# Kernel tuning notes

Hardware: AMD Instinct MI355X
Metric: run time of the kernel (lower is better)

Reference implementation:

```python
import jax, jax.numpy as jnp
import numpy as np

H = 90          # hidden size
T = 240         # timesteps
F = 180         # encoder input features (3*60)


def _lstmcell_zero_state(x, W_ih, b_ih, b_hh):
    """nn.LSTMCell applied with h0=c0=0 (as in the original loops).
    x: [..., in_feat]; W_ih: [4H, in_feat]. Gate order i,f,g,o (PyTorch)."""
    gates = jnp.einsum('btf,gf->btg', x, W_ih) + b_ih + b_hh  # [B,T,4H]
    i, f, g, o = jnp.split(gates, 4, axis=-1)
    c = jax.nn.sigmoid(i) * jnp.tanh(g)          # f * c0 term vanishes (c0=0)
    return jax.nn.sigmoid(o) * jnp.tanh(c)       # h'


def setup_inputs() -> dict:
    key = jax.random.key(0)
    ks = jax.random.split(key, 9)
    s_enc = 1.0 / np.sqrt(H)
    inp = {
        'x': jax.random.normal(ks[0], (1024, 3, 60, T), dtype=jnp.float32),
        'enc_W_ih': jax.random.uniform(ks[1], (4 * H, F), jnp.float32, -s_enc, s_enc),
        'enc_b_ih': jax.random.uniform(ks[2], (4 * H,), jnp.float32, -s_enc, s_enc),
        'enc_b_hh': jax.random.uniform(ks[3], (4 * H,), jnp.float32, -s_enc, s_enc),
        'dec_W_ih': jax.random.uniform(ks[4], (4 * H, H), jnp.float32, -s_enc, s_enc),
        'dec_b_ih': jax.random.uniform(ks[5], (4 * H,), jnp.float32, -s_enc, s_enc),
        'dec_b_hh': jax.random.uniform(ks[6], (4 * H,), jnp.float32, -s_enc, s_enc),
        'out_W': jax.random.uniform(ks[7], (40, T * H), jnp.float32, -1.0 / np.sqrt(T * H), 1.0 / np.sqrt(T * H)),
        'out_b': jax.random.uniform(ks[8], (40,), jnp.float32, -1.0 / np.sqrt(T * H), 1.0 / np.sqrt(T * H)),
    }
    return inp


def reference(x, enc_W_ih, enc_b_ih, enc_b_hh, dec_W_ih, dec_b_ih, dec_b_hh, out_W, out_b):
    # Encoder: [B,3,60,240] -> [B,240,180]
    xe = jnp.transpose(x, (0, 3, 1, 2)).reshape(-1, T, F)
    h1 = jax.nn.sigmoid(_lstmcell_zero_state(xe, enc_W_ih, enc_b_ih, enc_b_hh))  # [B,T,90]
    # Decoder: per-step LSTMCell (also zero-state each step)
    h2 = _lstmcell_zero_state(h1, dec_W_ih, dec_b_ih, dec_b_hh)  # [B,T,90]
    out = h2.reshape(-1, T * H) @ out_W.T + out_b                # [B,40]
    out = out.reshape(-1, 4, 10)
    return jax.nn.softmax(out, axis=2)
```

## Files before the change

kernel.cpp:

```cpp
#include <hip/hip_runtime.h>
#include <hip/hip_bf16.h>

#define TT 240
#define FEAT 180
#define HID 90

typedef __attribute__((ext_vector_type(8))) short bf16x8;
typedef __attribute__((ext_vector_type(4))) short s16x4;
typedef __attribute__((ext_vector_type(4))) float f32x4;

static __device__ __forceinline__ short f2bf(float f) {
    union { float f; unsigned int u; } c; c.f = f;
    return (short)((c.u + 0x8000u) >> 16);
}
static __device__ __forceinline__ float fexp2(float x) { return __builtin_amdgcn_exp2f(x); }
static __device__ __forceinline__ float frcp(float x)  { return __builtin_amdgcn_rcpf(x); }
#define LOG2E 1.4426950408889634f
static __device__ __forceinline__ float sigm(float x)  { return frcp(1.f + fexp2(-LOG2E * x)); }
static __device__ __forceinline__ float tanh_(float x) { return 2.f * frcp(1.f + fexp2(-2.f * LOG2E * x)) - 1.f; }
static __device__ __forceinline__ unsigned int pk2(float lo, float hi) {
    return (unsigned int)(unsigned short)f2bf(lo) | ((unsigned int)(unsigned short)f2bf(hi) << 16);
}

__global__ __launch_bounds__(256) void k_prep(
    const float* __restrict__ outW, const float* __restrict__ encW,
    const float* __restrict__ decW,
    short* __restrict__ woutB, short* __restrict__ wencP, short* __restrict__ wdecP)
{
    int idx = blockIdx.x * 256 + threadIdx.x;
    if (idx < 129600) {
        int row = idx / 2700, v = idx - row * 2700;
        uint4 w = {0u, 0u, 0u, 0u};
        if (row < 40) {
            const float* s = outW + row * 21600 + v * 8;
            f32x4 a = *(const f32x4*)(s);
            f32x4 b = *(const f32x4*)(s + 4);
            w.x = pk2(a[0], a[1]); w.y = pk2(a[2], a[3]);
            w.z = pk2(b[0], b[1]); w.w = pk2(b[2], b[3]);
        }
        *(uint4*)(woutB + row * 21600 + v * 8) = w;
        return;
    }
    idx -= 129600;
    if (idx < 288 * 192) {
        int row = idx / 192, k = idx - row * 192;
        int gi = row / 96, h = row - gi * 96;
        float v = 0.f;
        if (h < 90 && k < 180) {
            int srow = (gi == 0 ? 0 : (gi == 1 ? 180 : 270)) + h;
            v = encW[srow * 180 + k];
        }
        wencP[idx] = f2bf(v);
        return;
    }
    idx -= 288 * 192;
    if (idx < 288 * 96) {
        int row = idx / 96, k = idx - row * 96;
        int gi = row / 96, h = row - gi * 96;
        float v = 0.f;
        if (h < 90 && k < 90) {
            int srow = (gi == 0 ? 0 : (gi == 1 ? 180 : 270)) + h;
            v = decW[srow * 90 + k];
        }
        wdecP[idx] = f2bf(v);
    }
}

__global__ __launch_bounds__(384) void k_ed(
    const float* __restrict__ x,
    const short* __restrict__ wencP, const short* __restrict__ wdecP,
    const float* __restrict__ eb_ih, const float* __restrict__ eb_hh,
    const float* __restrict__ db_ih, const float* __restrict__ db_hh,
    short* __restrict__ h2)
{
    __shared__ short As[64][200];
    const int tid  = threadIdx.x;
    const int lane = tid & 63;
    const int wv   = tid >> 6;
    const int b    = blockIdx.x >> 2;
    const int q    = blockIdx.x & 3;
    const int r15  = lane & 15;
    const int k8   = lane >> 4;
    const int rbase = k8 * 4;

    bf16x8 wfE[3][6];
    #pragma unroll
    for (int g = 0; g < 3; ++g) {
        const short* wp = wencP + (g * 96 + wv * 16 + r15) * 192 + k8 * 8;
        #pragma unroll
        for (int kk = 0; kk < 6; ++kk) wfE[g][kk] = *(const bf16x8*)(wp + kk * 32);
    }
    const int h  = wv * 16 + r15;
    const int hc = (h < 90) ? h : 89;
    const float bIe = eb_ih[hc] + eb_hh[hc];
    const float bGe = eb_ih[180 + hc] + eb_hh[180 + hc];
    const float bOe = eb_ih[270 + hc] + eb_hh[270 + hc];
    const float bId = db_ih[hc] + db_hh[hc];
    const float bGd = db_ih[180 + hc] + db_hh[180 + hc];
    const float bOd = db_ih[270 + hc] + db_hh[270 + hc];

    {
        int row = tid / 6, u = tid - row * 6;
        *(unsigned int*)(&As[row][180 + u * 2]) = 0u;
        if (tid < 360) {
            int r = 60 + tid / 90, c2 = (tid - (tid / 90) * 90) * 2;
            *(unsigned int*)(&As[r][c2]) = 0u;
        }
    }

    {
        const float* xs = x + b * 43200 + q * 60;
        #pragma unroll
        for (int it = 0; it < 2; ++it) {
            int task = tid + 384 * it;
            if (task < 675) {
                int fb = task / 15, v = task - fb * 15;
                const float* p = xs + (fb * 4) * 240 + v * 4;
                f32x4 L0 = *(const f32x4*)(p);
                f32x4 L1 = *(const f32x4*)(p + 240);
                f32x4 L2 = *(const f32x4*)(p + 480);
                f32x4 L3 = *(const f32x4*)(p + 720);
                #pragma unroll
                for (int i = 0; i < 4; ++i) {
                    s16x4 w = { f2bf(L0[i]), f2bf(L1[i]), f2bf(L2[i]), f2bf(L3[i]) };
                    *(s16x4*)(&As[v * 4 + i][fb * 4]) = w;
                }
            }
        }
    }
    __syncthreads();

    short h1v[16];
    #pragma unroll
    for (int rs = 0; rs < 4; ++rs) {
        f32x4 aI = {0.f,0.f,0.f,0.f}, aG = {0.f,0.f,0.f,0.f}, aO = {0.f,0.f,0.f,0.f};
        #pragma unroll
        for (int kk = 0; kk < 6; ++kk) {
            bf16x8 a = *(const bf16x8*)(&As[rs * 16 + r15][kk * 32 + k8 * 8]);
            aI = __builtin_amdgcn_mfma_f32_16x16x32_bf16(a, wfE[0][kk], aI, 0, 0, 0);
            aG = __builtin_amdgcn_mfma_f32_16x16x32_bf16(a, wfE[1][kk], aG, 0, 0, 0);
            aO = __builtin_amdgcn_mfma_f32_16x16x32_bf16(a, wfE[2][kk], aO, 0, 0, 0);
        }
        #pragma unroll
        for (int rg = 0; rg < 4; ++rg) {
            float c  = sigm(aI[rg] + bIe) * tanh_(aG[rg] + bGe);
            float hv = sigm(aO[rg] + bOe) * tanh_(c);
            h1v[rs * 4 + rg] = f2bf(sigm(hv));
        }
    }
    __syncthreads();

    #pragma unroll
    for (int j = 0; j < 16; ++j)
        As[(j >> 2) * 16 + rbase + (j & 3)][h] = h1v[j];

    bf16x8 wfD[3][3];
    #pragma unroll
    for (int g = 0; g < 3; ++g) {
        const short* wp = wdecP + (g * 96 + wv * 16 + r15) * 96 + k8 * 8;
        #pragma unroll
        for (int kk = 0; kk < 3; ++kk) wfD[g][kk] = *(const bf16x8*)(wp + kk * 32);
    }
    __syncthreads();

    short h2v[16];
    #pragma unroll
    for (int rs = 0; rs < 4; ++rs) {
        f32x4 aI = {0.f,0.f,0.f,0.f}, aG = {0.f,0.f,0.f,0.f}, aO = {0.f,0.f,0.f,0.f};
        #pragma unroll
        for (int kk = 0; kk < 3; ++kk) {
            bf16x8 a = *(const bf16x8*)(&As[rs * 16 + r15][kk * 32 + k8 * 8]);
            aI = __builtin_amdgcn_mfma_f32_16x16x32_bf16(a, wfD[0][kk], aI, 0, 0, 0);
            aG = __builtin_amdgcn_mfma_f32_16x16x32_bf16(a, wfD[1][kk], aG, 0, 0, 0);
            aO = __builtin_amdgcn_mfma_f32_16x16x32_bf16(a, wfD[2][kk], aO, 0, 0, 0);
        }
        #pragma unroll
        for (int rg = 0; rg < 4; ++rg) {
            float c  = sigm(aI[rg] + bId) * tanh_(aG[rg] + bGd);
            float o2 = sigm(aO[rg] + bOd) * tanh_(c);
            h2v[rs * 4 + rg] = f2bf(o2);
        }
    }
    __syncthreads();

    short* h2s = &As[0][0];
    #pragma unroll
    for (int j = 0; j < 16; ++j)
        h2s[((j >> 2) * 16 + rbase + (j & 3)) * 96 + h] = h2v[j];
    __syncthreads();

    unsigned int* hp = (unsigned int*)(h2 + (size_t)b * 21600 + q * 5400);
    #pragma unroll
    for (int i = 0; i < 8; ++i) {
        int idx = tid + 384 * i;
        if (idx < 2700) {
            int r = idx / 45, c = idx - r * 45;
            hp[idx] = *(const unsigned int*)(&h2s[r * 96 + c * 2]);
        }
    }
}

#define KSPLIT 45
#define KST    15
__global__ __launch_bounds__(256) void k_out(
    const short* __restrict__ h2, const short* __restrict__ woutB,
    float* __restrict__ part, int B)
{
    __shared__ short Bs[48][488];
    const int MT  = B >> 6;
    const int bid = blockIdx.x;
    const int kc  = bid / MT;
    const int mt  = bid - kc * MT;
    const int tid = threadIdx.x;

    {
        const int k0 = kc * 480;
        #pragma unroll
        for (int j = 0; j < 12; ++j) {
            int g = tid + 256 * j;
            if (g < 2880) {
                int r = g / 60, c = g - r * 60;
                *(uint4*)(&Bs[r][c * 8]) =
                    *(const uint4*)(woutB + (size_t)r * 21600 + k0 + c * 8);
            }
        }
    }
    __syncthreads();

    const int w = tid >> 6, lane = tid & 63;
    const int r15 = lane & 15, k8 = lane >> 4;
    const int row = mt * 64 + w * 16 + r15;
    const short* aB = h2 + (size_t)row * 21600 + kc * 480 + k8 * 8;

    f32x4 a0 = {0.f,0.f,0.f,0.f}, a1 = {0.f,0.f,0.f,0.f}, a2 = {0.f,0.f,0.f,0.f};
    #pragma unroll 5
    for (int ks = 0; ks < KST; ++ks) {
        bf16x8 a  = *(const bf16x8*)(aB + ks * 32);
        bf16x8 q0 = *(const bf16x8*)(&Bs[r15][ks * 32 + k8 * 8]);
        bf16x8 q1 = *(const bf16x8*)(&Bs[16 + r15][ks * 32 + k8 * 8]);
        bf16x8 q2 = *(const bf16x8*)(&Bs[32 + r15][ks * 32 + k8 * 8]);
        a0 = __builtin_amdgcn_mfma_f32_16x16x32_bf16(a, q0, a0, 0, 0, 0);
        a1 = __builtin_amdgcn_mfma_f32_16x16x32_bf16(a, q1, a1, 0, 0, 0);
        a2 = __builtin_amdgcn_mfma_f32_16x16x32_bf16(a, q2, a2, 0, 0, 0);
    }
    float* pb = part + ((size_t)kc * B + mt * 64 + w * 16) * 48;
    #pragma unroll
    for (int rg = 0; rg < 4; ++rg) {
        int r = k8 * 4 + rg;
        pb[r * 48 +      r15] = a0[rg];
        pb[r * 48 + 16 + r15] = a1[rg];
        pb[r * 48 + 32 + r15] = a2[rg];
    }
}

__global__ __launch_bounds__(256) void k_soft(
    const float* __restrict__ part, const float* __restrict__ outb,
    float* __restrict__ out, int B)
{
    const int b = blockIdx.x, tid = threadIdx.x;
    __shared__ float psum[240];
    __shared__ float vals[40];
    if (tid < 240) {
        int o = tid % 40, g = tid / 40;
        float s = 0.f;
        for (int kc = g; kc < KSPLIT; kc += 6)
            s += part[((size_t)kc * B + b) * 48 + o];
        psum[tid] = s;
    }
    __syncthreads();
    if (tid < 40) {
        float s = outb[tid];
        #pragma unroll
        for (int g = 0; g < 6; ++g) s += psum[tid + 40 * g];
        vals[tid] = s;
    }
    __syncthreads();
    if (tid < 4) {
        float mx = -1e30f;
        #pragma unroll
        for (int j = 0; j < 10; ++j) mx = fmaxf(mx, vals[tid * 10 + j]);
        float e[10], s = 0.f;
        #pragma unroll
        for (int j = 0; j < 10; ++j) { e[j] = fexp2(LOG2E * (vals[tid * 10 + j] - mx)); s += e[j]; }
        float inv = frcp(s);
        #pragma unroll
        for (int j = 0; j < 10; ++j) out[b * 40 + tid * 10 + j] = e[j] * inv;
    }
}

extern "C" void kernel_launch(void* const* d_in, const int* in_sizes, int n_in,
                              void* d_out, int out_size, void* d_ws, size_t ws_size,
                              hipStream_t stream)
{
    const float* x     = (const float*)d_in[0];
    const float* encW  = (const float*)d_in[1];
    const float* eb_ih = (const float*)d_in[2];
    const float* eb_hh = (const float*)d_in[3];
    const float* decW  = (const float*)d_in[4];
    const float* db_ih = (const float*)d_in[5];
    const float* db_hh = (const float*)d_in[6];
    const float* outW  = (const float*)d_in[7];
    const float* outb  = (const float*)d_in[8];
    float* out = (float*)d_out;

    const int B = in_sizes[0] / (3 * 60 * TT);

    char* ws = (char*)d_ws;
    short* woutB = (short*)ws;
    short* wencP = (short*)(ws + 2073600);
    short* wdecP = (short*)(ws + 2184192);
    short* h2    = (short*)(ws + 2239488);
    float* part  = (float*)(ws + 2239488 + (size_t)B * 43200);

    k_prep<<<dim3(831), dim3(256), 0, stream>>>(outW, encW, decW, woutB, wencP, wdecP);
    k_ed<<<dim3(B * 4), dim3(384), 0, stream>>>(x, wencP, wdecP, eb_ih, eb_hh,
                                                db_ih, db_hh, h2);
    k_out<<<dim3(KSPLIT * (B >> 6)), dim3(256), 0, stream>>>(h2, woutB, part, B);
    k_soft<<<dim3(B), dim3(256), 0, stream>>>(part, outb, out, B);
}
```

Measured before the change: 361.1 us.

## Make encoder-decoder kernel persistent per batch with double-buffered x staging

k_ed now runs one block per batch element instead of four. It loops over the four 60-step quarters, double-buffering the x tile in LDS so the next quarter's global loads overlap decoder compute, and loads the encoder and decoder weight fragments into registers only once. Decoder outputs are written straight to global memory instead of going through an LDS staging pass. Other changes: hardware v_cvt_pk_bf16_f32 packing, full unroll of the k_out loop, and a vectorised split-K reduction in k_soft. The cost is fewer blocks, which reduces parallelism, plus doubled LDS and higher register pressure.

```diff
diff --git a/kernel.cpp b/kernel.cpp
--- a/kernel.cpp
+++ b/kernel.cpp
@@ -2,25 +2,24 @@
 #include <hip/hip_bf16.h>
 
 #define TT 240
-#define FEAT 180
-#define HID 90
 
 typedef __attribute__((ext_vector_type(8))) short bf16x8;
-typedef __attribute__((ext_vector_type(4))) short s16x4;
 typedef __attribute__((ext_vector_type(4))) float f32x4;
 
 static __device__ __forceinline__ short f2bf(float f) {
     union { float f; unsigned int u; } c; c.f = f;
     return (short)((c.u + 0x8000u) >> 16);
+}
+static __device__ __forceinline__ unsigned int cvtpk(float lo, float hi) {
+    unsigned int r;
+    asm("v_cvt_pk_bf16_f32 %0, %1, %2" : "=v"(r) : "v"(lo), "v"(hi));
+    return r;
 }
 static __device__ __forceinline__ float fexp2(float x) { return __builtin_amdgcn_exp2f(x); }
 static __device__ __forceinline__ float frcp(float x)  { return __builtin_amdgcn_rcpf(x); }
 #define LOG2E 1.4426950408889634f
 static __device__ __forceinline__ float sigm(float x)  { return frcp(1.f + fexp2(-LOG2E * x)); }
 static __device__ __forceinline__ float tanh_(float x) { return 2.f * frcp(1.f + fexp2(-2.f * LOG2E * x)) - 1.f; }
-static __device__ __forceinline__ unsigned int pk2(float lo, float hi) {
-    return (unsigned int)(unsigned short)f2bf(lo) | ((unsigned int)(unsigned short)f2bf(hi) << 16);
-}
 
 __global__ __launch_bounds__(256) void k_prep(
     const float* __restrict__ outW, const float* __restrict__ encW,
@@ -35,8 +34,8 @@
             const float* s = outW + row * 21600 + v * 8;
             f32x4 a = *(const f32x4*)(s);
             f32x4 b = *(const f32x4*)(s + 4);
-            w.x = pk2(a[0], a[1]); w.y = pk2(a[2], a[3]);
-            w.z = pk2(b[0], b[1]); w.w = pk2(b[2], b[3]);
+            w.x = cvtpk(a[0], a[1]); w.y = cvtpk(a[2], a[3]);
+            w.z = cvtpk(b[0], b[1]); w.w = cvtpk(b[2], b[3]);
         }
         *(uint4*)(woutB + row * 21600 + v * 8) = w;
         return;
@@ -66,19 +65,53 @@
     }
 }
 
-__global__ __launch_bounds__(384) void k_ed(
+static __device__ __forceinline__ void stage_tile(
+    const float* __restrict__ xq, short (*__restrict__ Xn)[200],
+    int fb1, int v1, int has2, int fb2, int v2)
+{
+    const float* p1 = xq + (fb1 * 4) * 240 + v1 * 4;
+    f32x4 A0 = *(const f32x4*)(p1);
+    f32x4 A1 = *(const f32x4*)(p1 + 240);
+    f32x4 A2 = *(const f32x4*)(p1 + 480);
+    f32x4 A3 = *(const f32x4*)(p1 + 720);
+    f32x4 B0, B1, B2, B3;
+    if (has2) {
+        const float* p2 = xq + (fb2 * 4) * 240 + v2 * 4;
+        B0 = *(const f32x4*)(p2);
+        B1 = *(const f32x4*)(p2 + 240);
+        B2 = *(const f32x4*)(p2 + 480);
+        B3 = *(const f32x4*)(p2 + 720);
+    }
+    #pragma unroll
+    for (int i = 0; i < 4; ++i) {
+        uint2 w;
+        w.x = cvtpk(A0[i], A1[i]);
+        w.y = cvtpk(A2[i], A3[i]);
+        *(uint2*)(&Xn[v1 * 4 + i][fb1 * 4]) = w;
+    }
+    if (has2) {
+        #pragma unroll
+        for (int i = 0; i < 4; ++i) {
+            uint2 w;
+            w.x = cvtpk(B0[i], B1[i]);
+            w.y = cvtpk(B2[i], B3[i]);
+            *(uint2*)(&Xn[v2 * 4 + i][fb2 * 4]) = w;
+        }
+    }
+}
+
+__global__ __launch_bounds__(384, 3) void k_ed(
     const float* __restrict__ x,
     const short* __restrict__ wencP, const short* __restrict__ wdecP,
     const float* __restrict__ eb_ih, const float* __restrict__ eb_hh,
     const float* __restrict__ db_ih, const float* __restrict__ db_hh,
     short* __restrict__ h2)
 {
-    __shared__ short As[64][200];
+    __shared__ short X[2][64][200];
     const int tid  = threadIdx.x;
     const int lane = tid & 63;
     const int wv   = tid >> 6;
-    const int b    = blockIdx.x >> 2;
-    const int q    = blockIdx.x & 3;
+    const int b    = blockIdx.x;
     const int r15  = lane & 15;
     const int k8   = lane >> 4;
     const int rbase = k8 * 4;
@@ -90,6 +123,14 @@
         #pragma unroll
         for (int kk = 0; kk < 6; ++kk) wfE[g][kk] = *(const bf16x8*)(wp + kk * 32);
     }
+    bf16x8 wfD[3][3];
+    #pragma unroll
+    for (int g = 0; g < 3; ++g) {
+        const short* wp = wdecP + (g * 96 + wv * 16 + r15) * 96 + k8 * 8;
+        #pragma unroll
+        for (int kk = 0; kk < 3; ++kk) wfD[g][kk] = *(const bf16x8*)(wp + kk * 32);
+    }
+
     const int h  = wv * 16 + r15;
     const int hc = (h < 90) ? h : 89;
     const float bIe = eb_ih[hc] + eb_hh[hc];
@@ -99,104 +140,84 @@
     const float bGd = db_ih[180 + hc] + db_hh[180 + hc];
     const float bOd = db_ih[270 + hc] + db_hh[270 + hc];
 
-    {
-        int row = tid / 6, u = tid - row * 6;
-        *(unsigned int*)(&As[row][180 + u * 2]) = 0u;
-        if (tid < 360) {
-            int r = 60 + tid / 90, c2 = (tid - (tid / 90) * 90) * 2;
-            *(unsigned int*)(&As[r][c2]) = 0u;
-        }
-    }
-
-    {
-        const float* xs = x + b * 43200 + q * 60;
-        #pragma unroll
-        for (int it = 0; it < 2; ++it) {
-            int task = tid + 384 * it;
-            if (task < 675) {
-                int fb = task / 15, v = task - fb * 15;
-                const float* p = xs + (fb * 4) * 240 + v * 4;
-                f32x4 L0 = *(const f32x4*)(p);
-                f32x4 L1 = *(const f32x4*)(p + 240);
-                f32x4 L2 = *(const f32x4*)(p + 480);
-                f32x4 L3 = *(const f32x4*)(p + 720);
+    for (int i = tid; i < 2000; i += 384) {
+        int bi = (i >= 1000);
+        int j  = i - bi * 1000;
+        if (j < 400) {
+            int r = j / 100, c = j - r * 100;
+            *(unsigned int*)(&X[bi][60 + r][c * 2]) = 0u;
+        } else {
+            int jj = j - 400;
+            int r = jj / 10, c = jj - r * 10;
+            *(unsigned int*)(&X[bi][r][180 + c * 2]) = 0u;
+        }
+    }
+
+    const int fb1 = tid / 15, v1 = tid - fb1 * 15;
+    const int has2 = (tid < 291);
+    const int t2 = tid + 384;
+    const int fb2 = t2 / 15, v2 = t2 - fb2 * 15;
+    const float* xb = x + (size_t)b * 43200;
+    short* h2g = h2 + (size_t)b * 21600;
+
+    stage_tile(xb, X[0], fb1, v1, has2, fb2, v2);
+
+    int p = 0;
+    #pragma unroll 1
+    for (int q = 0; q < 4; ++q) {
+        __syncthreads();
+        short (*Xc)[200] = X[p];
+
+        short h1v[16];
+        #pragma unroll
+        for (int rs = 0; rs < 4; ++rs) {
+            f32x4 aI = {0.f,0.f,0.f,0.f}, aG = {0.f,0.f,0.f,0.f}, aO = {0.f,0.f,0.f,0.f};
+            #pragma unroll
+            for (int kk = 0; kk < 6; ++kk) {
+                bf16x8 a = *(const bf16x8*)(&Xc[rs * 16 + r15][kk * 32 + k8 * 8]);
+                aI = __builtin_amdgcn_mfma_f32_16x16x32_bf16(a, wfE[0][kk], aI, 0, 0, 0);
+                aG = __builtin_amdgcn_mfma_f32_16x16x32_bf16(a, wfE[1][kk], aG, 0, 0, 0);
+                aO = __builtin_amdgcn_mfma_f32_16x16x32_bf16(a, wfE[2][kk], aO, 0, 0, 0);
+            }
+            #pragma unroll
+            for (int rg = 0; rg < 4; ++rg) {
+                float c  = sigm(aI[rg] + bIe) * tanh_(aG[rg] + bGe);
+                float hv = sigm(aO[rg] + bOe) * tanh_(c);
+                h1v[rs * 4 + rg] = f2bf(sigm(hv));
+            }
+        }
+        __syncthreads();
+
+        #pragma unroll
+        for (int j = 0; j < 16; ++j)
+            Xc[(j >> 2) * 16 + rbase + (j & 3)][h] = h1v[j];
+
+        if (q < 3)
+            stage_tile(xb + (q + 1) * 60, X[p ^ 1], fb1, v1, has2, fb2, v2);
+
+        __syncthreads();
+
+        #pragma unroll
+        for (int rs = 0; rs < 4; ++rs) {
+            f32x4 aI = {0.f,0.f,0.f,0.f}, aG = {0.f,0.f,0.f,0.f}, aO = {0.f,0.f,0.f,0.f};
+            #pragma unroll
+            for (int kk = 0; kk < 3; ++kk) {
+                bf16x8 a = *(const bf16x8*)(&Xc[rs * 16 + r15][kk * 32 + k8 * 8]);
+                aI = __builtin_amdgcn_mfma_f32_16x16x32_bf16(a, wfD[0][kk], aI, 0, 0, 0);
+                aG = __builtin_amdgcn_mfma_f32_16x16x32_bf16(a, wfD[1][kk], aG, 0, 0, 0);
+                aO = __builtin_amdgcn_mfma_f32_16x16x32_bf16(a, wfD[2][kk], aO, 0, 0, 0);
+            }
+            if (h < 90) {
                 #pragma unroll
-                for (int i = 0; i < 4; ++i) {
-                    s16x4 w = { f2bf(L0[i]), f2bf(L1[i]), f2bf(L2[i]), f2bf(L3[i]) };
-                    *(s16x4*)(&As[v * 4 + i][fb * 4]) = w;
+                for (int rg = 0; rg < 4; ++rg) {
+                    int row = rs * 16 + rbase + rg;
+                    float c  = sigm(aI[rg] + bId) * tanh_(aG[rg] + bGd);
+                    float o2 = sigm(aO[rg] + bOd) * tanh_(c);
+                    if (row < 60) h2g[q * 5400 + row * 90 + h] = f2bf(o2);
                 }
             }
         }
-    }
-    __syncthreads();
-
-    short h1v[16];
-    #pragma unroll
-    for (int rs = 0; rs < 4; ++rs) {
-        f32x4 aI = {0.f,0.f,0.f,0.f}, aG = {0.f,0.f,0.f,0.f}, aO = {0.f,0.f,0.f,0.f};
-        #pragma unroll
-        for (int kk = 0; kk < 6; ++kk) {
-            bf16x8 a = *(const bf16x8*)(&As[rs * 16 + r15][kk * 32 + k8 * 8]);
-            aI = __builtin_amdgcn_mfma_f32_16x16x32_bf16(a, wfE[0][kk], aI, 0, 0, 0);
-            aG = __builtin_amdgcn_mfma_f32_16x16x32_bf16(a, wfE[1][kk], aG, 0, 0, 0);
-            aO = __builtin_amdgcn_mfma_f32_16x16x32_bf16(a, wfE[2][kk], aO, 0, 0, 0);
-        }
-        #pragma unroll
-        for (int rg = 0; rg < 4; ++rg) {
-            float c  = sigm(aI[rg] + bIe) * tanh_(aG[rg] + bGe);
-            float hv = sigm(aO[rg] + bOe) * tanh_(c);
-            h1v[rs * 4 + rg] = f2bf(sigm(hv));
-        }
-    }
-    __syncthreads();
-
-    #pragma unroll
-    for (int j = 0; j < 16; ++j)
-        As[(j >> 2) * 16 + rbase + (j & 3)][h] = h1v[j];
-
-    bf16x8 wfD[3][3];
-    #pragma unroll
-    for (int g = 0; g < 3; ++g) {
-        const short* wp = wdecP + (g * 96 + wv * 16 + r15) * 96 + k8 * 8;
-        #pragma unroll
-        for (int kk = 0; kk < 3; ++kk) wfD[g][kk] = *(const bf16x8*)(wp + kk * 32);
-    }
-    __syncthreads();
-
-    short h2v[16];
-    #pragma unroll
-    for (int rs = 0; rs < 4; ++rs) {
-        f32x4 aI = {0.f,0.f,0.f,0.f}, aG = {0.f,0.f,0.f,0.f}, aO = {0.f,0.f,0.f,0.f};
-        #pragma unroll
-        for (int kk = 0; kk < 3; ++kk) {
-            bf16x8 a = *(const bf16x8*)(&As[rs * 16 + r15][kk * 32 + k8 * 8]);
-            aI = __builtin_amdgcn_mfma_f32_16x16x32_bf16(a, wfD[0][kk], aI, 0, 0, 0);
-            aG = __builtin_amdgcn_mfma_f32_16x16x32_bf16(a, wfD[1][kk], aG, 0, 0, 0);
-            aO = __builtin_amdgcn_mfma_f32_16x16x32_bf16(a, wfD[2][kk], aO, 0, 0, 0);
-        }
-        #pragma unroll
-        for (int rg = 0; rg < 4; ++rg) {
-            float c  = sigm(aI[rg] + bId) * tanh_(aG[rg] + bGd);
-            float o2 = sigm(aO[rg] + bOd) * tanh_(c);
-            h2v[rs * 4 + rg] = f2bf(o2);
-        }
-    }
-    __syncthreads();
-
-    short* h2s = &As[0][0];
-    #pragma unroll
-    for (int j = 0; j < 16; ++j)
-        h2s[((j >> 2) * 16 + rbase + (j & 3)) * 96 + h] = h2v[j];
-    __syncthreads();
-
-    unsigned int* hp = (unsigned int*)(h2 + (size_t)b * 21600 + q * 5400);
-    #pragma unroll
-    for (int i = 0; i < 8; ++i) {
-        int idx = tid + 384 * i;
-        if (idx < 2700) {
-            int r = idx / 45, c = idx - r * 45;
-            hp[idx] = *(const unsigned int*)(&h2s[r * 96 + c * 2]);
-        }
+        p ^= 1;
     }
 }
 
@@ -233,7 +254,7 @@
     const short* aB = h2 + (size_t)row * 21600 + kc * 480 + k8 * 8;
 
     f32x4 a0 = {0.f,0.f,0.f,0.f}, a1 = {0.f,0.f,0.f,0.f}, a2 = {0.f,0.f,0.f,0.f};
-    #pragma unroll 5
+    #pragma unroll
     for (int ks = 0; ks < KST; ++ks) {
         bf16x8 a  = *(const bf16x8*)(aB + ks * 32);
         bf16x8 q0 = *(const bf16x8*)(&Bs[r15][ks * 32 + k8 * 8]);
@@ -258,21 +279,25 @@
     float* __restrict__ out, int B)
 {
     const int b = blockIdx.x, tid = threadIdx.x;
-    __shared__ float psum[240];
-    __shared__ float vals[40];
-    if (tid < 240) {
-        int o = tid % 40, g = tid / 40;
-        float s = 0.f;
-        for (int kc = g; kc < KSPLIT; kc += 6)
-            s += part[((size_t)kc * B + b) * 48 + o];
-        psum[tid] = s;
+    __shared__ f32x4 red[16][12];
+    __shared__ float vals[48];
+    if (tid < 192) {
+        int j = tid / 12, g = tid - j * 12;
+        f32x4 s = {0.f, 0.f, 0.f, 0.f};
+        for (int kc = j; kc < KSPLIT; kc += 16)
+            s += *(const f32x4*)(part + ((size_t)kc * B + b) * 48 + g * 4);
+        red[j][g] = s;
     }
     __syncthreads();
-    if (tid < 40) {
-        float s = outb[tid];
-        #pragma unroll
-        for (int g = 0; g < 6; ++g) s += psum[tid + 40 * g];
-        vals[tid] = s;
+    if (tid < 12) {
+        f32x4 s = red[0][tid];
+        #pragma unroll
+        for (int j = 1; j < 16; ++j) s += red[j][tid];
+        #pragma unroll
+        for (int e = 0; e < 4; ++e) {
+            int o = tid * 4 + e;
+            vals[o] = s[e] + ((o < 40) ? outb[o] : 0.f);
+        }
     }
     __syncthreads();
     if (tid < 4) {
@@ -313,8 +338,8 @@
     float* part  = (float*)(ws + 2239488 + (size_t)B * 43200);
 
     k_prep<<<dim3(831), dim3(256), 0, stream>>>(outW, encW, decW, woutB, wencP, wdecP);
-    k_ed<<<dim3(B * 4), dim3(384), 0, stream>>>(x, wencP, wdecP, eb_ih, eb_hh,
-                                                db_ih, db_hh, h2);
+    k_ed<<<dim3(B), dim3(384), 0, stream>>>(x, wencP, wdecP, eb_ih, eb_hh,
+                                            db_ih, db_hh, h2);
     k_out<<<dim3(KSPLIT * (B >> 6)), dim3(256), 0, stream>>>(h2, woutB, part, B);
     k_soft<<<dim3(B), dim3(256), 0, stream>>>(part, outb, out, B);
 }
```

Result: slower. 374.0 us (+3.6%).
